# Kernel optimization log

Measured on AMD Instinct MI355X. Metric: run time of the kernel, lower is better.

## Reference

```python
import jax, jax.numpy as jnp
import numpy as np


def setup_inputs() -> dict:
    key = jax.random.key(0)
    k1, k2, k3, k4 = jax.random.split(key, 4)
    B, N, D, P = 1, 8192, 128, 2  # batch must be 1 (see .view(B,N,N) in source)
    x = jax.random.normal(k1, (B, N, D), dtype=jnp.float32)
    points = jax.random.normal(k2, (B, N, P), dtype=jnp.float32)
    # nn.Linear params, stored as (in, out) so y = x @ W + b
    W1 = jax.random.normal(k3, (2 * D, 2 * D), dtype=jnp.float32) * 0.04
    b1 = jnp.zeros((2 * D,), dtype=jnp.float32)
    W2 = jax.random.normal(k4, (2 * D, D), dtype=jnp.float32) * 0.04
    b2 = jnp.zeros((D,), dtype=jnp.float32)
    return {"x": x, "points": points, "W1": W1, "b1": b1, "W2": W2, "b2": b2, "K": 16}


def reference(x, points, W1, b1, W2, b2, K):
    B, N, _ = points.shape
    D = x.shape[-1]
    # torch.cdist on flattened (B*N, P) points, reshaped to (B, N, N)
    # (valid only for B == 1, matching the original module). Squared distance
    # is monotone in Euclidean distance, so top-k indices are identical.
    pf = points.reshape(B * N, -1)
    sq = jnp.sum(pf * pf, axis=-1)
    d2 = sq[:, None] + sq[None, :] - 2.0 * (pf @ pf.T)  # (BN, BN)
    d2 = d2.reshape(B, N, N)
    # topk(-dist, K+1) -> nearest K+1 (self first), drop self
    _, idx = jax.lax.top_k(-d2, K + 1)  # (B, N, K+1)
    idx = idx[:, :, 1:]  # (B, N, K)
    # gather neighbor features: knn_fts[b, n, k] = x[b, idx[b, n, k]]
    knn = x[jnp.arange(B)[:, None, None], idx]  # (B, N, K, D)
    center = jnp.broadcast_to(x[:, :, None, :], (B, N, K, D))
    local = jnp.concatenate([knn - center, center], axis=-1)  # (B, N, K, 2D)
    h = jax.nn.gelu(local @ W1 + b1, approximate=False)
    h = jax.nn.gelu(h @ W2 + b2, approximate=False)
    return jnp.mean(h, axis=2)  # (B, N, D)
```

## Files before the change

kernel.cpp:

```cpp
#include <hip/hip_runtime.h>

typedef __attribute__((ext_vector_type(8))) short short8;
typedef __attribute__((ext_vector_type(4))) float f32x4;

__device__ __forceinline__ unsigned short f2bf(float f) {
    unsigned int u = __float_as_uint(f);
    unsigned int r = u + 0x7fffu + ((u >> 16) & 1u);
    return (unsigned short)(r >> 16);
}

__device__ __forceinline__ float bf2f(short s) {
    return __uint_as_float(((unsigned int)(unsigned short)s) << 16);
}

__device__ __forceinline__ float gelu_fast(float v) {
    float x2 = v * v;
    float s  = v * fmaf(-0.102943195f, x2, -2.3022077f);
    float e  = __builtin_amdgcn_exp2f(s);
    return v * __builtin_amdgcn_rcpf(1.0f + e);
}

__device__ __forceinline__ unsigned int d2key(float d2) {
    unsigned int u = __float_as_uint(d2);
    return u ^ (((unsigned int)(((int)u) >> 31)) | 0x80000000u);
}

#define U64MAX 0xFFFFFFFFFFFFFFFFull

#define D2_FROM_Q(px, py, XI, YI, SQI)                                           \
    ({ const float sqj_ = __fadd_rn(__fmul_rn((px), (px)), __fmul_rn((py), (py))); \
       const float t_   = fmaf((YI), (py), __fmul_rn((XI), (px)));                 \
       const float s_   = __fadd_rn((SQI), sqj_);                                  \
       fmaf(-2.0f, t_, s_); })

__device__ __forceinline__ unsigned long long bitonic64(unsigned long long v, int lane) {
#pragma unroll
    for (int k = 2; k <= 64; k <<= 1) {
#pragma unroll
        for (int j = k >> 1; j > 0; j >>= 1) {
            unsigned long long pv = __shfl_xor(v, j, 64);
            const bool up  = ((lane & k) == 0);
            const bool low = ((lane & j) == 0);
            const unsigned long long mn = (v < pv) ? v : pv;
            const unsigned long long mx = (v < pv) ? pv : v;
            v = (up == low) ? mn : mx;
        }
    }
    return v;
}

__device__ __forceinline__ float bitonic64f(float v, int lane) {
#pragma unroll
    for (int k = 2; k <= 64; k <<= 1) {
#pragma unroll
        for (int j = k >> 1; j > 0; j >>= 1) {
            float pv = __shfl_xor(v, j, 64);
            const bool up  = ((lane & k) == 0);
            const bool low = ((lane & j) == 0);
            const float mn = fminf(v, pv);
            const float mx = fmaxf(v, pv);
            v = (up == low) ? mn : mx;
        }
    }
    return v;
}

__device__ __forceinline__ void insert_cand(
        unsigned long long* crow, int* cnt,
        float px, float py, float XI, float YI, float SQI, int i) {
    const float d2 = D2_FROM_Q(px, py, XI, YI, SQI);
    const unsigned int key = d2key(d2);
    int pos = atomicAdd(cnt, 1);
    if (pos < 128)
        crow[pos] = ((unsigned long long)key << 32) | (unsigned int)i;
}

#define KNN_SLACK 2.0e-3f

__global__ __launch_bounds__(256) void knn_kernel(
        const float* __restrict__ points,
        const float* __restrict__ W1, const float* __restrict__ W2,
        unsigned short* __restrict__ W1t, unsigned short* __restrict__ W2t,
        int* __restrict__ idx_out) {
    __shared__ float pmin[4][4][64];
    __shared__ float tshr[4];
    __shared__ unsigned long long cand[4][128];
    __shared__ int ccnt[4];

    const int bid = blockIdx.x;
    const int tid = threadIdx.x;

    if (bid < 384) {
        int g = bid * 256 + tid;
        if (g < 65536) {
            int d = g >> 8, c = g & 255;
            W1t[c * 256 + d] = f2bf(W1[g]);
        } else if (g < 98304) {
            int g2 = g - 65536;
            int d = g2 >> 7, c = g2 & 127;
            W2t[c * 256 + d] = f2bf(W2[g2]);
        }
        return;
    }

    const int wv    = tid >> 6;
    const int lane  = tid & 63;
    const int qbase = (bid - 384) << 2;

    float xi[4], yi[4], sqi_[4], n2x[4], n2y[4];
#pragma unroll
    for (int t = 0; t < 4; ++t) {
        xi[t] = points[(qbase + t) * 2 + 0];
        yi[t] = points[(qbase + t) * 2 + 1];
        sqi_[t] = __fadd_rn(__fmul_rn(xi[t], xi[t]), __fmul_rn(yi[t], yi[t]));
        n2x[t] = -2.0f * xi[t];
        n2y[t] = -2.0f * yi[t];
    }

    const float4* p4 = (const float4*)points;
    const float4* pw = p4 + wv * 1024 + lane;

    if (tid < 4) ccnt[tid] = 0;

    float vmn[4] = {1e30f, 1e30f, 1e30f, 1e30f};
#pragma unroll 4
    for (int j = 0; j < 16; ++j) {
        const float4 pp = pw[j * 64];
        const float sqa = fmaf(pp.x, pp.x, pp.y * pp.y);
        const float sqb = fmaf(pp.z, pp.z, pp.w * pp.w);
#pragma unroll
        for (int t = 0; t < 4; ++t) {
            const float da = fmaf(n2x[t], pp.x, fmaf(n2y[t], pp.y, sqa));
            const float db = fmaf(n2x[t], pp.z, fmaf(n2y[t], pp.w, sqb));
            vmn[t] = fminf(fminf(da, db), vmn[t]);
        }
    }
#pragma unroll
    for (int t = 0; t < 4; ++t) pmin[t][wv][lane] = vmn[t];
    __syncthreads();

    {
        const int q = wv;
        const float m = fminf(fminf(pmin[q][0][lane], pmin[q][1][lane]),
                              fminf(pmin[q][2][lane], pmin[q][3][lane]));
        const float s = bitonic64f(m, lane);
        if (lane == 16) tshr[q] = s + KNN_SLACK;
    }
    __syncthreads();
    float Ta[4];
#pragma unroll
    for (int t = 0; t < 4; ++t) Ta[t] = tshr[t];

#pragma unroll 4
    for (int j = 0; j < 16; ++j) {
        const float4 pp = pw[j * 64];
        const int i0 = (wv * 1024 + j * 64 + lane) * 2;
        const float sqa = fmaf(pp.x, pp.x, pp.y * pp.y);
        const float sqb = fmaf(pp.z, pp.z, pp.w * pp.w);
#pragma unroll
        for (int t = 0; t < 4; ++t) {
            const float da = fmaf(n2x[t], pp.x, fmaf(n2y[t], pp.y, sqa));
            const float db = fmaf(n2x[t], pp.z, fmaf(n2y[t], pp.w, sqb));
            if (da <= Ta[t])
                insert_cand(cand[t], &ccnt[t],
                            pp.x, pp.y, xi[t], yi[t], sqi_[t], i0);
            if (db <= Ta[t])
                insert_cand(cand[t], &ccnt[t],
                            pp.z, pp.w, xi[t], yi[t], sqi_[t], i0 + 1);
        }
    }
    __syncthreads();

    {
        const int q = qbase + wv;
        unsigned long long* candw = cand[wv];
        const int cc = ccnt[wv];
        const int n = cc < 128 ? cc : 128;
        if (n <= 64) {
            unsigned long long v0 = (lane < n) ? candw[lane] : U64MAX;
            v0 = bitonic64(v0, lane);
            if (lane >= 1 && lane <= 16)
                idx_out[q * 16 + lane - 1] = (int)(unsigned int)(v0 & 0xFFFFFFFFull);
        } else {
            unsigned long long v0 = (lane < n)      ? candw[lane]      : U64MAX;
            unsigned long long v1 = (lane + 64 < n) ? candw[lane + 64] : U64MAX;
#pragma unroll 1
            for (int pick = 0; pick < 17; ++pick) {
                unsigned long long m = (v0 < v1) ? v0 : v1;
#pragma unroll
                for (int d = 1; d < 64; d <<= 1) {
                    unsigned long long pm = __shfl_xor(m, d, 64);
                    m = (pm < m) ? pm : m;
                }
                if (pick > 0 && lane == 0)
                    idx_out[q * 16 + pick - 1] = (int)(unsigned int)(m & 0xFFFFFFFFull);
                if (v0 == m) v0 = U64MAX;
                else if (v1 == m) v1 = U64MAX;
            }
        }
    }
}

__global__ __launch_bounds__(256) void gemmAD_kernel(
        const float* __restrict__ x, const unsigned short* __restrict__ W1t,
        const float* __restrict__ b1,
        unsigned short* __restrict__ Abf, unsigned short* __restrict__ Dbf) {
    __shared__ unsigned short sx[64 * 136];
    const int tid = threadIdx.x;
    const int rb  = (blockIdx.x >> 1) * 64;
    const int cb  = (blockIdx.x & 1) * 128;

    {
        const int r   = ((tid >> 6) << 4) | (tid & 15);
        const int seg = (tid >> 4) & 3;
        const float* xr = x + (rb + r) * 128 + seg * 32;
        unsigned short* dst = sx + r * 136 + seg * 32;
#pragma unroll
        for (int u = 0; u < 8; ++u) {
            float4 a = ((const float4*)xr)[u];
            uint2 w;
            w.x = (unsigned)f2bf(a.x) | ((unsigned)f2bf(a.y) << 16);
            w.y = (unsigned)f2bf(a.z) | ((unsigned)f2bf(a.w) << 16);
            *(uint2*)(dst + u * 4) = w;
        }
    }
    __syncthreads();

    const int lane = tid & 63, wv = tid >> 6;
    const int m = lane & 15, quad = lane >> 4;
    const int ko0 = quad * 8;

    f32x4 accA[8], accC[8];
#pragma unroll
    for (int i = 0; i < 8; ++i) { accA[i] = (f32x4){0,0,0,0}; accC[i] = (f32x4){0,0,0,0}; }

#pragma unroll
    for (int ks = 0; ks < 4; ++ks) {
        const int ko = ks * 32 + ko0;
        short8 af[4], bA[2], bC[2];
#pragma unroll
        for (int rt = 0; rt < 4; ++rt)
            af[rt] = *(const short8*)(sx + (rt * 16 + m) * 136 + ko);
#pragma unroll
        for (int ct = 0; ct < 2; ++ct) {
            const unsigned short* wp = W1t + (cb + wv * 32 + ct * 16 + m) * 256 + ko;
            bA[ct] = *(const short8*)(wp);
            bC[ct] = *(const short8*)(wp + 128);
        }
#pragma unroll
        for (int rt = 0; rt < 4; ++rt)
#pragma unroll
            for (int ct = 0; ct < 2; ++ct) {
                accA[rt * 2 + ct] = __builtin_amdgcn_mfma_f32_16x16x32_bf16(
                    af[rt], bA[ct], accA[rt * 2 + ct], 0, 0, 0);
                accC[rt * 2 + ct] = __builtin_amdgcn_mfma_f32_16x16x32_bf16(
                    af[rt], bC[ct], accC[rt * 2 + ct], 0, 0, 0);
            }
    }

#pragma unroll
    for (int ct = 0; ct < 2; ++ct) {
        const int col = cb + wv * 32 + ct * 16 + m;
        const float bias = b1[col];
#pragma unroll
        for (int rt = 0; rt < 4; ++rt)
#pragma unroll
            for (int j = 0; j < 4; ++j) {
                const int row = rb + rt * 16 + quad * 4 + j;
                float a = accA[rt * 2 + ct][j];
                float d = accC[rt * 2 + ct][j] - a + bias;
                Abf[row * 256 + col] = f2bf(a);
                Dbf[row * 256 + col] = f2bf(d);
            }
    }
}

__global__ __launch_bounds__(256) void mlp_kernel(
        const unsigned short* __restrict__ Abf, const unsigned short* __restrict__ Dbf,
        const unsigned short* __restrict__ W2t, const float* __restrict__ b2,
        const int* __restrict__ idx, float* __restrict__ out) {
    __shared__ unsigned short sh[64 * 264];
    const int tid = threadIdx.x;
    const int qb  = blockIdx.x << 2;

    {
        const int r   = ((tid >> 6) << 4) | (tid & 15);
        const int seg = (tid >> 4) & 3;
        const int gq  = qb + (r >> 4);
        const int nb  = idx[(gq << 4) + (r & 15)];
        const unsigned short* arow = Abf + nb * 256 + seg * 64;
        const unsigned short* drow = Dbf + gq * 256 + seg * 64;
        unsigned short* dst = sh + r * 264 + seg * 64;
#pragma unroll
        for (int u = 0; u < 8; ++u) {
            short8 av = *(const short8*)(arow + u * 8);
            short8 dv = *(const short8*)(drow + u * 8);
            short8 hv;
#pragma unroll
            for (int e = 0; e < 8; ++e) {
                float h = bf2f(av[e]) + bf2f(dv[e]);
                hv[e] = (short)f2bf(gelu_fast(h));
            }
            *(short8*)(dst + u * 8) = hv;
        }
    }
    __syncthreads();

    const int lane = tid & 63, wv = tid >> 6;
    const int m = lane & 15, quad = lane >> 4;
    const int ko0 = quad * 8;

    f32x4 acc2[8];
#pragma unroll
    for (int i = 0; i < 8; ++i) acc2[i] = (f32x4){0.f, 0.f, 0.f, 0.f};
#pragma unroll
    for (int ks = 0; ks < 8; ++ks) {
        const int ko = ks * 32 + ko0;
        short8 af[4], bfr[2];
#pragma unroll
        for (int rt = 0; rt < 4; ++rt)
            af[rt] = *(const short8*)(sh + (rt * 16 + m) * 264 + ko);
#pragma unroll
        for (int ct = 0; ct < 2; ++ct)
            bfr[ct] = *(const short8*)(W2t + (wv * 32 + ct * 16 + m) * 256 + ko);
#pragma unroll
        for (int rt = 0; rt < 4; ++rt)
#pragma unroll
            for (int ct = 0; ct < 2; ++ct)
                acc2[rt * 2 + ct] = __builtin_amdgcn_mfma_f32_16x16x32_bf16(
                    af[rt], bfr[ct], acc2[rt * 2 + ct], 0, 0, 0);
    }

#pragma unroll
    for (int ct = 0; ct < 2; ++ct) {
        const int col = wv * 32 + ct * 16 + m;
        const float bias = b2[col];
#pragma unroll
        for (int rt = 0; rt < 4; ++rt) {
            float s = 0.f;
#pragma unroll
            for (int j = 0; j < 4; ++j)
                s += gelu_fast(acc2[rt * 2 + ct][j] + bias);
            s += __shfl_xor(s, 16, 64);
            s += __shfl_xor(s, 32, 64);
            if (quad == 0) out[(qb + rt) * 128 + col] = s * 0.0625f;
        }
    }
}

extern "C" void kernel_launch(void* const* d_in, const int* in_sizes, int n_in,
                              void* d_out, int out_size, void* d_ws, size_t ws_size,
                              hipStream_t stream) {
    const float* x      = (const float*)d_in[0];
    const float* points = (const float*)d_in[1];
    const float* W1     = (const float*)d_in[2];
    const float* b1     = (const float*)d_in[3];
    const float* W2     = (const float*)d_in[4];
    const float* b2     = (const float*)d_in[5];
    float* out = (float*)d_out;

    char* ws = (char*)d_ws;
    unsigned short* W1t = (unsigned short*)ws;
    unsigned short* W2t = (unsigned short*)(ws + 131072);
    int*            idx = (int*)(ws + 196608);
    unsigned short* Abf = (unsigned short*)(ws + 720896);
    unsigned short* Dbf = (unsigned short*)(ws + 4915200);

    knn_kernel<<<2432, 256, 0, stream>>>(points, W1, W2, W1t, W2t, idx);
    gemmAD_kernel<<<256, 256, 0, stream>>>(x, W1t, b1, Abf, Dbf);
    mlp_kernel<<<2048, 256, 0, stream>>>(Abf, Dbf, W2t, b2, idx, out);
}
```

Before: 131.4 us.

## Widen kNN blocks to 8 queries and stage GEMM output through LDS

The kNN kernel now runs 512-thread blocks that each handle 8 queries. Each wave scans an eighth of the points, so every point load is shared by twice as many queries, and half as many blocks are launched. The first GEMM now uses 64-column tiles with twice as many blocks. Its bf16 results are written to shared memory and then stored to global memory with coalesced 16-byte writes, replacing the scattered 2-byte stores. The cost is more registers per kNN thread, more LDS per block, and an extra barrier in the GEMM.

```diff
diff --git a/kernel.cpp b/kernel.cpp
--- a/kernel.cpp
+++ b/kernel.cpp
@@ -77,25 +77,25 @@
 
 #define KNN_SLACK 2.0e-3f
 
-__global__ __launch_bounds__(256) void knn_kernel(
+__global__ __launch_bounds__(512) void knn_kernel(
         const float* __restrict__ points,
         const float* __restrict__ W1, const float* __restrict__ W2,
         unsigned short* __restrict__ W1t, unsigned short* __restrict__ W2t,
         int* __restrict__ idx_out) {
-    __shared__ float pmin[4][4][64];
-    __shared__ float tshr[4];
-    __shared__ unsigned long long cand[4][128];
-    __shared__ int ccnt[4];
+    __shared__ float pmin[8][8][64];
+    __shared__ float tshr[8];
+    __shared__ unsigned long long cand[8][128];
+    __shared__ int ccnt[8];
 
     const int bid = blockIdx.x;
     const int tid = threadIdx.x;
 
-    if (bid < 384) {
-        int g = bid * 256 + tid;
+    if (bid < 192) {
+        int g = bid * 512 + tid;
         if (g < 65536) {
             int d = g >> 8, c = g & 255;
             W1t[c * 256 + d] = f2bf(W1[g]);
-        } else if (g < 98304) {
+        } else {
             int g2 = g - 65536;
             int d = g2 >> 7, c = g2 & 127;
             W2t[c * 256 + d] = f2bf(W2[g2]);
@@ -105,11 +105,11 @@
 
     const int wv    = tid >> 6;
     const int lane  = tid & 63;
-    const int qbase = (bid - 384) << 2;
-
-    float xi[4], yi[4], sqi_[4], n2x[4], n2y[4];
-#pragma unroll
-    for (int t = 0; t < 4; ++t) {
+    const int qbase = (bid - 192) << 3;
+
+    float xi[8], yi[8], sqi_[8], n2x[8], n2y[8];
+#pragma unroll
+    for (int t = 0; t < 8; ++t) {
         xi[t] = points[(qbase + t) * 2 + 0];
         yi[t] = points[(qbase + t) * 2 + 1];
         sqi_[t] = __fadd_rn(__fmul_rn(xi[t], xi[t]), __fmul_rn(yi[t], yi[t]));
@@ -118,47 +118,47 @@
     }
 
     const float4* p4 = (const float4*)points;
-    const float4* pw = p4 + wv * 1024 + lane;
-
-    if (tid < 4) ccnt[tid] = 0;
-
-    float vmn[4] = {1e30f, 1e30f, 1e30f, 1e30f};
-#pragma unroll 4
-    for (int j = 0; j < 16; ++j) {
+    const float4* pw = p4 + wv * 512 + lane;
+
+    if (tid < 8) ccnt[tid] = 0;
+
+    float vmn[8] = {1e30f, 1e30f, 1e30f, 1e30f, 1e30f, 1e30f, 1e30f, 1e30f};
+#pragma unroll
+    for (int j = 0; j < 8; ++j) {
         const float4 pp = pw[j * 64];
         const float sqa = fmaf(pp.x, pp.x, pp.y * pp.y);
         const float sqb = fmaf(pp.z, pp.z, pp.w * pp.w);
 #pragma unroll
-        for (int t = 0; t < 4; ++t) {
+        for (int t = 0; t < 8; ++t) {
             const float da = fmaf(n2x[t], pp.x, fmaf(n2y[t], pp.y, sqa));
             const float db = fmaf(n2x[t], pp.z, fmaf(n2y[t], pp.w, sqb));
             vmn[t] = fminf(fminf(da, db), vmn[t]);
         }
     }
 #pragma unroll
-    for (int t = 0; t < 4; ++t) pmin[t][wv][lane] = vmn[t];
-    __syncthreads();
-
-    {
-        const int q = wv;
-        const float m = fminf(fminf(pmin[q][0][lane], pmin[q][1][lane]),
-                              fminf(pmin[q][2][lane], pmin[q][3][lane]));
+    for (int t = 0; t < 8; ++t) pmin[t][wv][lane] = vmn[t];
+    __syncthreads();
+
+    {
+        float m = pmin[wv][0][lane];
+#pragma unroll
+        for (int w = 1; w < 8; ++w) m = fminf(m, pmin[wv][w][lane]);
         const float s = bitonic64f(m, lane);
-        if (lane == 16) tshr[q] = s + KNN_SLACK;
-    }
-    __syncthreads();
-    float Ta[4];
-#pragma unroll
-    for (int t = 0; t < 4; ++t) Ta[t] = tshr[t];
-
-#pragma unroll 4
-    for (int j = 0; j < 16; ++j) {
+        if (lane == 16) tshr[wv] = s + KNN_SLACK;
+    }
+    __syncthreads();
+    float Ta[8];
+#pragma unroll
+    for (int t = 0; t < 8; ++t) Ta[t] = tshr[t];
+
+#pragma unroll
+    for (int j = 0; j < 8; ++j) {
         const float4 pp = pw[j * 64];
-        const int i0 = (wv * 1024 + j * 64 + lane) * 2;
+        const int i0 = (wv * 512 + j * 64 + lane) * 2;
         const float sqa = fmaf(pp.x, pp.x, pp.y * pp.y);
         const float sqb = fmaf(pp.z, pp.z, pp.w * pp.w);
 #pragma unroll
-        for (int t = 0; t < 4; ++t) {
+        for (int t = 0; t < 8; ++t) {
             const float da = fmaf(n2x[t], pp.x, fmaf(n2y[t], pp.y, sqa));
             const float db = fmaf(n2x[t], pp.z, fmaf(n2y[t], pp.w, sqb));
             if (da <= Ta[t])
@@ -206,9 +206,11 @@
         const float* __restrict__ b1,
         unsigned short* __restrict__ Abf, unsigned short* __restrict__ Dbf) {
     __shared__ unsigned short sx[64 * 136];
+    __shared__ unsigned short tA[64 * 68];
+    __shared__ unsigned short tD[64 * 68];
     const int tid = threadIdx.x;
-    const int rb  = (blockIdx.x >> 1) * 64;
-    const int cb  = (blockIdx.x & 1) * 128;
+    const int rb  = (blockIdx.x >> 2) * 64;
+    const int cb  = (blockIdx.x & 3) * 64;
 
     {
         const int r   = ((tid >> 6) << 4) | (tid & 15);
@@ -230,48 +232,55 @@
     const int m = lane & 15, quad = lane >> 4;
     const int ko0 = quad * 8;
 
-    f32x4 accA[8], accC[8];
-#pragma unroll
-    for (int i = 0; i < 8; ++i) { accA[i] = (f32x4){0,0,0,0}; accC[i] = (f32x4){0,0,0,0}; }
+    f32x4 accA[4], accC[4];
+#pragma unroll
+    for (int i = 0; i < 4; ++i) { accA[i] = (f32x4){0,0,0,0}; accC[i] = (f32x4){0,0,0,0}; }
+
+    const int colL = wv * 16 + m;
 
 #pragma unroll
     for (int ks = 0; ks < 4; ++ks) {
         const int ko = ks * 32 + ko0;
-        short8 af[4], bA[2], bC[2];
+        short8 af[4];
 #pragma unroll
         for (int rt = 0; rt < 4; ++rt)
             af[rt] = *(const short8*)(sx + (rt * 16 + m) * 136 + ko);
-#pragma unroll
-        for (int ct = 0; ct < 2; ++ct) {
-            const unsigned short* wp = W1t + (cb + wv * 32 + ct * 16 + m) * 256 + ko;
-            bA[ct] = *(const short8*)(wp);
-            bC[ct] = *(const short8*)(wp + 128);
-        }
+        const unsigned short* wp = W1t + (cb + colL) * 256 + ko;
+        const short8 bA = *(const short8*)(wp);
+        const short8 bC = *(const short8*)(wp + 128);
+#pragma unroll
+        for (int rt = 0; rt < 4; ++rt) {
+            accA[rt] = __builtin_amdgcn_mfma_f32_16x16x32_bf16(af[rt], bA, accA[rt], 0, 0, 0);
+            accC[rt] = __builtin_amdgcn_mfma_f32_16x16x32_bf16(af[rt], bC, accC[rt], 0, 0, 0);
+        }
+    }
+
+    {
+        const float bias = b1[cb + colL];
 #pragma unroll
         for (int rt = 0; rt < 4; ++rt)
 #pragma unroll
-            for (int ct = 0; ct < 2; ++ct) {
-                accA[rt * 2 + ct] = __builtin_amdgcn_mfma_f32_16x16x32_bf16(
-                    af[rt], bA[ct], accA[rt * 2 + ct], 0, 0, 0);
-                accC[rt * 2 + ct] = __builtin_amdgcn_mfma_f32_16x16x32_bf16(
-                    af[rt], bC[ct], accC[rt * 2 + ct], 0, 0, 0);
+            for (int j = 0; j < 4; ++j) {
+                const int rowL = rt * 16 + quad * 4 + j;
+                float a = accA[rt][j];
+                float d = accC[rt][j] - a + bias;
+                tA[rowL * 68 + colL] = f2bf(a);
+                tD[rowL * 68 + colL] = f2bf(d);
             }
     }
-
-#pragma unroll
-    for (int ct = 0; ct < 2; ++ct) {
-        const int col = cb + wv * 32 + ct * 16 + m;
-        const float bias = b1[col];
-#pragma unroll
-        for (int rt = 0; rt < 4; ++rt)
-#pragma unroll
-            for (int j = 0; j < 4; ++j) {
-                const int row = rb + rt * 16 + quad * 4 + j;
-                float a = accA[rt * 2 + ct][j];
-                float d = accC[rt * 2 + ct][j] - a + bias;
-                Abf[row * 256 + col] = f2bf(a);
-                Dbf[row * 256 + col] = f2bf(d);
-            }
+    __syncthreads();
+
+    {
+        const int r  = tid >> 2;
+        const int sg = tid & 3;
+        const unsigned short* sa = tA + r * 68 + sg * 16;
+        const unsigned short* sd = tD + r * 68 + sg * 16;
+        unsigned short* da = Abf + (rb + r) * 256 + cb + sg * 16;
+        unsigned short* dd = Dbf + (rb + r) * 256 + cb + sg * 16;
+        *(short8*)(da)     = *(const short8*)(sa);
+        *(short8*)(da + 8) = *(const short8*)(sa + 8);
+        *(short8*)(dd)     = *(const short8*)(sd);
+        *(short8*)(dd + 8) = *(const short8*)(sd + 8);
     }
 }
 
@@ -366,7 +375,7 @@
     unsigned short* Abf = (unsigned short*)(ws + 720896);
     unsigned short* Dbf = (unsigned short*)(ws + 4915200);
 
-    knn_kernel<<<2432, 256, 0, stream>>>(points, W1, W2, W1t, W2t, idx);
-    gemmAD_kernel<<<256, 256, 0, stream>>>(x, W1t, b1, Abf, Dbf);
+    knn_kernel<<<1216, 512, 0, stream>>>(points, W1, W2, W1t, W2t, idx);
+    gemmAD_kernel<<<512, 256, 0, stream>>>(x, W1t, b1, Abf, Dbf);
     mlp_kernel<<<2048, 256, 0, stream>>>(Abf, Dbf, W2t, b2, idx, out);
 }
```

After: 135.6 us. 3.2% more time.
